# Kernel tuning notes

Measured on AMD Instinct MI355X. Metric: run time of the kernel, lower is better.

The kernel has to match this reference:

```python
import jax, jax.numpy as jnp
import numpy as np

IN_F = 4096
OUT_F = 4096
GS = 128              # group_size
GC = IN_F // GS       # group_count = 32
PACK = 8              # int4 values per int32


def setup_inputs() -> dict:
    key = jax.random.key(0)
    k1, k2, k3, k4, k5 = jax.random.split(key, 5)
    x = jax.random.normal(k1, (4, 2048, IN_F), dtype=jnp.float32)
    # packed int4 weights: (out_features, in_features // 8), nibbles in low->high bits
    qweight = jax.random.randint(k2, (OUT_F, IN_F // PACK), -(2**31), 2**31 - 1, dtype=jnp.int32)
    scales = jax.random.uniform(k3, (GC, OUT_F), dtype=jnp.float32) * 0.01
    qzeros = jax.random.randint(k4, (GC, OUT_F), 0, 16, dtype=jnp.int32)
    bias = jax.random.normal(k5, (OUT_F,), dtype=jnp.float32) * 0.01
    return {"x": x, "qweight": qweight, "scales": scales, "qzeros": qzeros, "bias": bias}


def _dequantize(qweight, scales, qzeros):
    # unpack 8 nibbles per int32 along last dim (shifts 0,4,...,28), as in _unpack_int4_last_dim
    shifts = jnp.arange(0, 32, 4, dtype=jnp.int32)  # [8]
    w_int = ((qweight[:, :, None] >> shifts) & 15)  # (OUT, IN//8, 8)
    w_int = w_int.reshape(OUT_F, IN_F).astype(jnp.float32)  # (OUT, IN)
    gid = jnp.arange(IN_F) // GS  # (IN,) group id per input channel
    z = qzeros.astype(jnp.float32)[gid].T   # (OUT, IN)
    s = scales[gid].T                        # (OUT, IN)
    return (w_int - z) * s                   # (OUT, IN)


def reference(x, qweight, scales, qzeros, bias):
    W = _dequantize(qweight, scales, qzeros)          # (OUT, IN)
    # F.linear: y = x @ W^T + b
    return jnp.einsum('bsi,oi->bso', x, W) + bias
```

## Files before the change

### kernel.cpp

```cpp
#include <hip/hip_runtime.h>
#include <hip/hip_bf16.h>
#include <stdint.h>

#define IN_F 4096
#define OUT_F 4096
#define M_TOTAL 8192
#define NKT 64

typedef __hip_bfloat16 bf16;
typedef __attribute__((ext_vector_type(8))) short bf16x8;
typedef __attribute__((ext_vector_type(4))) float f32x4;

__global__ __launch_bounds__(256) void dequant_w(const int* __restrict__ qweight,
                                                 const float* __restrict__ scales,
                                                 const int* __restrict__ qzeros,
                                                 bf16* __restrict__ Wb) {
    int idx = blockIdx.x * 256 + threadIdx.x;
    int o = idx >> 9;
    int j = idx & 511;
    int g = j >> 4;
    int qw = qweight[idx];
    float s = scales[g * OUT_F + o];
    float z = (float)qzeros[g * OUT_F + o];
    union { bf16 h[8]; uint4 q; } out;
#pragma unroll
    for (int b = 0; b < 8; ++b) {
        float w = (float)((qw >> (4 * b)) & 15);
        out.h[b] = __float2bfloat16((w - z) * s);
    }
    *reinterpret_cast<uint4*>(Wb + ((size_t)o * IN_F + j * 8)) = out.q;
}

__global__ __launch_bounds__(256) void cvt_x(const float* __restrict__ x,
                                             bf16* __restrict__ Xb, int n8) {
    int idx = blockIdx.x * 256 + threadIdx.x;
    if (idx >= n8) return;
    const float4* p = reinterpret_cast<const float4*>(x) + (size_t)idx * 2;
    float4 a = p[0], b = p[1];
    union { bf16 h[8]; uint4 q; } o;
    o.h[0] = __float2bfloat16(a.x); o.h[1] = __float2bfloat16(a.y);
    o.h[2] = __float2bfloat16(a.z); o.h[3] = __float2bfloat16(a.w);
    o.h[4] = __float2bfloat16(b.x); o.h[5] = __float2bfloat16(b.y);
    o.h[6] = __float2bfloat16(b.z); o.h[7] = __float2bfloat16(b.w);
    reinterpret_cast<uint4*>(Xb)[idx] = o.q;
}


__device__ __forceinline__ void gload16(const bf16* g, char* l) {
    __builtin_amdgcn_global_load_lds(
        (const __attribute__((address_space(1))) void*)g,
        (__attribute__((address_space(3))) void*)l, 16, 0, 0);
}

__device__ __forceinline__ void stage_half(const bf16* __restrict__ Gt,
                                           char* ldsb, int wave, int lane) {
    const int slog8 = ((lane & 7) ^ (lane >> 3)) * 8;
#pragma unroll
    for (int j = 0; j < 2; ++j) {
        int r = wave * 16 + j * 8 + (lane >> 3);
        gload16(Gt + (size_t)r * IN_F + slog8, ldsb + (wave * 2 + j) * 1024);
    }
}

#define BARRIER() do { asm volatile("" ::: "memory"); \
                       __builtin_amdgcn_s_barrier();  \
                       asm volatile("" ::: "memory"); } while (0)
#define LGKM0()   asm volatile("s_waitcnt lgkmcnt(0)" ::: "memory")
#define VMCNT4()  asm volatile("s_waitcnt vmcnt(4)" ::: "memory")
#define VMCNT0()  asm volatile("s_waitcnt vmcnt(0)" ::: "memory")

#define LDA_SET(DST, BUF, MH) do {                                              \
  _Pragma("unroll") for (int m4 = 0; m4 < 4; ++m4)                              \
  _Pragma("unroll") for (int kk = 0; kk < 2; ++kk)                              \
    DST[m4][kk] = *reinterpret_cast<const bf16x8*>(sm + (BUF) * 65536           \
        + ((wr * 128 + (MH) * 64 + m4 * 16 + l15) << 7)                         \
        + ((((kk << 2) + lq) ^ l7) << 4));                                      \
} while (0)

#define LDB_SET(BUF, NH) do {                                                   \
  _Pragma("unroll") for (int n2 = 0; n2 < 2; ++n2)                              \
  _Pragma("unroll") for (int kk = 0; kk < 2; ++kk)                              \
    bfr[n2][kk] = *reinterpret_cast<const bf16x8*>(sm + (BUF) * 65536 + 32768   \
        + ((wc * 64 + (NH) * 32 + n2 * 16 + l15) << 7)                          \
        + ((((kk << 2) + lq) ^ l7) << 4));                                      \
} while (0)

#define MMA_Q(AF, MH, NH) do {                                                  \
  __builtin_amdgcn_s_setprio(1);                                                \
  _Pragma("unroll") for (int m4 = 0; m4 < 4; ++m4)                              \
  _Pragma("unroll") for (int n2 = 0; n2 < 2; ++n2)                              \
  _Pragma("unroll") for (int kk = 0; kk < 2; ++kk)                              \
    acc[(MH) * 4 + m4][(NH) * 2 + n2] = __builtin_amdgcn_mfma_f32_16x16x32_bf16(\
        AF[m4][kk], bfr[n2][kk], acc[(MH) * 4 + m4][(NH) * 2 + n2], 0, 0, 0);   \
  __builtin_amdgcn_s_setprio(0);                                                \
} while (0)

__global__ __launch_bounds__(512, 2) void gemm256(const bf16* __restrict__ A,
                                                  const bf16* __restrict__ B,
                                                  const float* __restrict__ bias,
                                                  float* __restrict__ C) {
    extern __shared__ char sm[];
    const int tid  = threadIdx.x;
    const int wave = tid >> 6;
    const int lane = tid & 63;
    const int wr   = wave >> 2;
    const int wc   = wave & 3;
    const int l15  = lane & 15;
    const int lq   = lane >> 4;
    const int l7   = lane & 7;

    const int nwg = gridDim.x;
    const int cpx = nwg >> 3;
    const int wg  = blockIdx.x;
    const int swz = (wg & 7) * cpx + (wg >> 3);
    const int bm  = swz >> 4;
    const int bn  = swz & 15;
    const int m0  = bm * 256;
    const int n0  = bn * 256;

    f32x4 acc[8][4];
#pragma unroll
    for (int m = 0; m < 8; ++m)
#pragma unroll
        for (int n = 0; n < 4; ++n) acc[m][n] = (f32x4){0.f, 0.f, 0.f, 0.f};

    bf16x8 af0[4][2], af1[4][2], bfr[2][2];

    stage_half(A + (size_t)m0 * IN_F,                sm + 0,     wave, lane);
    stage_half(A + (size_t)(m0 + 128) * IN_F,        sm + 16384, wave, lane);
    stage_half(B + (size_t)n0 * IN_F,                sm + 32768, wave, lane);
    stage_half(B + (size_t)(n0 + 128) * IN_F,        sm + 49152, wave, lane);
    stage_half(A + (size_t)m0 * IN_F + 64,           sm + 65536, wave, lane);
    stage_half(A + (size_t)(m0 + 128) * IN_F + 64,   sm + 81920, wave, lane);
    VMCNT4();
    BARRIER();

    for (int i = 0; i < 32; ++i) {
        const int tB1 = 2 * i + 1;
        const int t2  = 2 * i + 2;
        const int t3  = 2 * i + 3;
        const bool g2 = t2 < NKT;
        const bool g3 = t3 < NKT;
        const bf16* Bk1 = B + (size_t)tB1 * 64;
        const bf16* Ak2 = A + (size_t)t2 * 64;
        const bf16* Bk2 = B + (size_t)t2 * 64;
        const bf16* Ak3 = A + (size_t)t3 * 64;

        LDA_SET(af0, 0, 0);
        LDB_SET(0, 0);
        stage_half(Bk1 + (size_t)n0 * IN_F,         sm + 98304,  wave, lane);
        BARRIER(); LGKM0();
        MMA_Q(af0, 0, 0);
        BARRIER();
        LDA_SET(af1, 0, 1);
        stage_half(Bk1 + (size_t)(n0 + 128) * IN_F, sm + 114688, wave, lane);
        BARRIER(); LGKM0();
        MMA_Q(af1, 1, 0);
        BARRIER();
        LDB_SET(0, 1);
        if (g2) stage_half(Ak2 + (size_t)m0 * IN_F,         sm + 0,     wave, lane);
        BARRIER(); LGKM0();
        MMA_Q(af0, 0, 1);
        BARRIER();
        if (g2) stage_half(Ak2 + (size_t)(m0 + 128) * IN_F, sm + 16384, wave, lane);
        BARRIER(); LGKM0();
        MMA_Q(af1, 1, 1);
        if (i < 31) { VMCNT4(); } else { VMCNT0(); }
        BARRIER();

        LDA_SET(af0, 1, 0);
        LDB_SET(1, 0);
        if (g2) stage_half(Bk2 + (size_t)n0 * IN_F,         sm + 32768, wave, lane);
        BARRIER(); LGKM0();
        MMA_Q(af0, 0, 0);
        BARRIER();
        LDA_SET(af1, 1, 1);
        if (g2) stage_half(Bk2 + (size_t)(n0 + 128) * IN_F, sm + 49152, wave, lane);
        BARRIER(); LGKM0();
        MMA_Q(af1, 1, 0);
        BARRIER();
        LDB_SET(1, 1);
        if (g3) stage_half(Ak3 + (size_t)m0 * IN_F,         sm + 65536, wave, lane);
        BARRIER(); LGKM0();
        MMA_Q(af0, 0, 1);
        BARRIER();
        if (g3) stage_half(Ak3 + (size_t)(m0 + 128) * IN_F, sm + 81920, wave, lane);
        BARRIER(); LGKM0();
        MMA_Q(af1, 1, 1);
        if (i < 31) { VMCNT4(); } else { VMCNT0(); }
        BARRIER();
    }

    const int crow0 = m0 + wr * 128 + lq * 4;
    const int ccol0 = n0 + wc * 64 + l15;
#pragma unroll
    for (int n = 0; n < 4; ++n) {
        float bv = bias[ccol0 + n * 16];
#pragma unroll
        for (int m = 0; m < 8; ++m)
#pragma unroll
            for (int r = 0; r < 4; ++r)
                C[(size_t)(crow0 + m * 16 + r) * OUT_F + ccol0 + n * 16] = acc[m][n][r] + bv;
    }
}

__global__ __launch_bounds__(256) void fallback_gemm(const float* __restrict__ x,
                                                     const int* __restrict__ qweight,
                                                     const float* __restrict__ scales,
                                                     const int* __restrict__ qzeros,
                                                     const float* __restrict__ bias,
                                                     float* __restrict__ out) {
    __shared__ float Asf[64][65];
    __shared__ float Bsf[64][65];
    int bm = blockIdx.x >> 6;
    int bn = blockIdx.x & 63;
    int m0 = bm * 64, n0 = bn * 64;
    int t  = threadIdx.x;
    int tr = t >> 4, tc = t & 15;
    float acc[4][4] = {};
    for (int kt = 0; kt < IN_F; kt += 64) {
#pragma unroll
        for (int i = 0; i < 4; ++i) {
            int idx = t + i * 256;
            int r = idx >> 4, c4 = idx & 15;
            float4 v = *reinterpret_cast<const float4*>(x + (size_t)(m0 + r) * IN_F + kt + c4 * 4);
            Asf[r][c4 * 4 + 0] = v.x; Asf[r][c4 * 4 + 1] = v.y;
            Asf[r][c4 * 4 + 2] = v.z; Asf[r][c4 * 4 + 3] = v.w;
        }
#pragma unroll
        for (int i = 0; i < 2; ++i) {
            int idx = t + i * 256;
            int r = idx >> 3, k8 = idx & 7;
            int kk = kt + k8 * 8;
            int o  = n0 + r;
            int qw = qweight[(size_t)o * (IN_F / 8) + (kk >> 3)];
            int g  = kk >> 7;
            float s = scales[g * OUT_F + o];
            float z = (float)qzeros[g * OUT_F + o];
#pragma unroll
            for (int b = 0; b < 8; ++b)
                Bsf[r][k8 * 8 + b] = ((float)((qw >> (4 * b)) & 15) - z) * s;
        }
        __syncthreads();
#pragma unroll 8
        for (int k = 0; k < 64; ++k) {
            float a[4], bb[4];
#pragma unroll
            for (int i = 0; i < 4; ++i) a[i] = Asf[tr * 4 + i][k];
#pragma unroll
            for (int j = 0; j < 4; ++j) bb[j] = Bsf[tc * 4 + j][k];
#pragma unroll
            for (int i = 0; i < 4; ++i)
#pragma unroll
                for (int j = 0; j < 4; ++j) acc[i][j] += a[i] * bb[j];
        }
        __syncthreads();
    }
#pragma unroll
    for (int i = 0; i < 4; ++i) {
        int row = m0 + tr * 4 + i;
#pragma unroll
        for (int j = 0; j < 4; ++j) {
            int col = n0 + tc * 4 + j;
            out[(size_t)row * OUT_F + col] = acc[i][j] + bias[col];
        }
    }
}

extern "C" void kernel_launch(void* const* d_in, const int* in_sizes, int n_in,
                              void* d_out, int out_size, void* d_ws, size_t ws_size,
                              hipStream_t stream) {
    (void)in_sizes; (void)n_in; (void)out_size;
    const float* x       = (const float*)d_in[0];
    const int*   qweight = (const int*)d_in[1];
    const float* scales  = (const float*)d_in[2];
    const int*   qzeros  = (const int*)d_in[3];
    const float* bias    = (const float*)d_in[4];
    float* out = (float*)d_out;

    const size_t needW = (size_t)OUT_F * IN_F * sizeof(bf16);
    const size_t needX = (size_t)M_TOTAL * IN_F * sizeof(bf16);

    if (ws_size >= needW + needX) {
        bf16* Wb = (bf16*)d_ws;
        bf16* Xb = (bf16*)((char*)d_ws + needW);
        dequant_w<<<(OUT_F * (IN_F / 8)) / 256, 256, 0, stream>>>(qweight, scales, qzeros, Wb);
        int n8 = M_TOTAL * IN_F / 8;
        cvt_x<<<(n8 + 255) / 256, 256, 0, stream>>>(x, Xb, n8);
        gemm256<<<(M_TOTAL / 256) * (OUT_F / 256), 512, 131072, stream>>>(Xb, Wb, bias, out);
    } else {
        fallback_gemm<<<(M_TOTAL / 64) * (OUT_F / 64), 256, 0, stream>>>(
            x, qweight, scales, qzeros, bias, out);
    }
}
```

Baseline: 274.3 us.

## Stage GEMM tiles by wave-quadrant units to prefetch deeper

Replaces half-tile staging with A/B staging units matched to which wave quadrant consumes them, so each load slot fills exactly the rows the next MMA phase reads. The prefetch schedule is reordered to issue loads further ahead (one extra unit in the prologue, vmcnt raised from 4 to 6), aiming to hide global-to-LDS latency behind MFMA work. The cost is more in-flight loads, and correctness depends on the new ordering of LDS buffer reuse.

```diff
diff --git a/kernel.cpp b/kernel.cpp
--- a/kernel.cpp
+++ b/kernel.cpp
@@ -52,13 +52,23 @@
         (__attribute__((address_space(3))) void*)l, 16, 0, 0);
 }
 
-__device__ __forceinline__ void stage_half(const bf16* __restrict__ Gt,
-                                           char* ldsb, int wave, int lane) {
+__device__ __forceinline__ void stage_Aunit(const bf16* __restrict__ G, char* Abase,
+                                            int MH, int wave, int lane) {
     const int slog8 = ((lane & 7) ^ (lane >> 3)) * 8;
 #pragma unroll
     for (int j = 0; j < 2; ++j) {
-        int r = wave * 16 + j * 8 + (lane >> 3);
-        gload16(Gt + (size_t)r * IN_F + slog8, ldsb + (wave * 2 + j) * 1024);
+        int rb = ((wave >> 2) << 7) + (MH << 6) + ((wave & 3) << 4) + (j << 3);
+        gload16(G + (size_t)(rb + (lane >> 3)) * IN_F + slog8, Abase + rb * 128);
+    }
+}
+
+__device__ __forceinline__ void stage_Bunit(const bf16* __restrict__ G, char* Bbase,
+                                            int NH, int wave, int lane) {
+    const int slog8 = ((lane & 7) ^ (lane >> 3)) * 8;
+#pragma unroll
+    for (int j = 0; j < 2; ++j) {
+        int rb = ((wave >> 1) << 6) + (NH << 5) + ((wave & 1) << 4) + (j << 3);
+        gload16(G + (size_t)(rb + (lane >> 3)) * IN_F + slog8, Bbase + rb * 128);
     }
 }
 
@@ -66,7 +76,7 @@
                        __builtin_amdgcn_s_barrier();  \
                        asm volatile("" ::: "memory"); } while (0)
 #define LGKM0()   asm volatile("s_waitcnt lgkmcnt(0)" ::: "memory")
-#define VMCNT4()  asm volatile("s_waitcnt vmcnt(4)" ::: "memory")
+#define VMCNT6()  asm volatile("s_waitcnt vmcnt(6)" ::: "memory")
 #define VMCNT0()  asm volatile("s_waitcnt vmcnt(0)" ::: "memory")
 
 #define LDA_SET(DST, BUF, MH) do {                                              \
@@ -118,6 +128,14 @@
     const int m0  = bm * 256;
     const int n0  = bn * 256;
 
+    const bf16* Arow = A + (size_t)m0 * IN_F;
+    const bf16* Brow = B + (size_t)n0 * IN_F;
+
+    char* buf0A = sm;
+    char* buf0B = sm + 32768;
+    char* buf1A = sm + 65536;
+    char* buf1B = sm + 98304;
+
     f32x4 acc[8][4];
 #pragma unroll
     for (int m = 0; m < 8; ++m)
@@ -126,68 +144,69 @@
 
     bf16x8 af0[4][2], af1[4][2], bfr[2][2];
 
-    stage_half(A + (size_t)m0 * IN_F,                sm + 0,     wave, lane);
-    stage_half(A + (size_t)(m0 + 128) * IN_F,        sm + 16384, wave, lane);
-    stage_half(B + (size_t)n0 * IN_F,                sm + 32768, wave, lane);
-    stage_half(B + (size_t)(n0 + 128) * IN_F,        sm + 49152, wave, lane);
-    stage_half(A + (size_t)m0 * IN_F + 64,           sm + 65536, wave, lane);
-    stage_half(A + (size_t)(m0 + 128) * IN_F + 64,   sm + 81920, wave, lane);
-    VMCNT4();
+    stage_Aunit(Arow,       buf0A, 0, wave, lane);
+    stage_Aunit(Arow,       buf0A, 1, wave, lane);
+    stage_Bunit(Brow,       buf0B, 0, wave, lane);
+    stage_Bunit(Brow,       buf0B, 1, wave, lane);
+    stage_Aunit(Arow + 64,  buf1A, 0, wave, lane);
+    stage_Aunit(Arow + 64,  buf1A, 1, wave, lane);
+    stage_Bunit(Brow + 64,  buf1B, 0, wave, lane);
+    VMCNT6();
     BARRIER();
 
     for (int i = 0; i < 32; ++i) {
-        const int tB1 = 2 * i + 1;
-        const int t2  = 2 * i + 2;
-        const int t3  = 2 * i + 3;
-        const bool g2 = t2 < NKT;
-        const bool g3 = t3 < NKT;
-        const bf16* Bk1 = B + (size_t)tB1 * 64;
-        const bf16* Ak2 = A + (size_t)t2 * 64;
-        const bf16* Bk2 = B + (size_t)t2 * 64;
-        const bf16* Ak3 = A + (size_t)t3 * 64;
+        const int t1 = 2 * i + 1;
+        const int t2 = 2 * i + 2;
+        const int t3 = 2 * i + 3;
+        const bool gg = (i < 31);
+        const bf16* At2 = Arow + t2 * 64;
+        const bf16* Bt2 = Brow + t2 * 64;
+        const bf16* At3 = Arow + t3 * 64;
+        const bf16* Bt1 = Brow + t1 * 64;
+        const bf16* Bt3 = Brow + t3 * 64;
 
         LDA_SET(af0, 0, 0);
         LDB_SET(0, 0);
-        stage_half(Bk1 + (size_t)n0 * IN_F,         sm + 98304,  wave, lane);
+        stage_Bunit(Bt1, buf1B, 1, wave, lane);
         BARRIER(); LGKM0();
         MMA_Q(af0, 0, 0);
         BARRIER();
         LDA_SET(af1, 0, 1);
-        stage_half(Bk1 + (size_t)(n0 + 128) * IN_F, sm + 114688, wave, lane);
+        if (gg) stage_Aunit(At2, buf0A, 0, wave, lane);
         BARRIER(); LGKM0();
         MMA_Q(af1, 1, 0);
         BARRIER();
         LDB_SET(0, 1);
-        if (g2) stage_half(Ak2 + (size_t)m0 * IN_F,         sm + 0,     wave, lane);
+        if (gg) stage_Aunit(At2, buf0A, 1, wave, lane);
         BARRIER(); LGKM0();
         MMA_Q(af0, 0, 1);
         BARRIER();
-        if (g2) stage_half(Ak2 + (size_t)(m0 + 128) * IN_F, sm + 16384, wave, lane);
+        if (gg) stage_Bunit(Bt2, buf0B, 0, wave, lane);
         BARRIER(); LGKM0();
         MMA_Q(af1, 1, 1);
-        if (i < 31) { VMCNT4(); } else { VMCNT0(); }
+        if (gg) { VMCNT6(); } else { VMCNT0(); }
         BARRIER();
 
         LDA_SET(af0, 1, 0);
         LDB_SET(1, 0);
-        if (g2) stage_half(Bk2 + (size_t)n0 * IN_F,         sm + 32768, wave, lane);
+        if (gg) stage_Bunit(Bt2, buf0B, 1, wave, lane);
         BARRIER(); LGKM0();
         MMA_Q(af0, 0, 0);
         BARRIER();
         LDA_SET(af1, 1, 1);
-        if (g2) stage_half(Bk2 + (size_t)(n0 + 128) * IN_F, sm + 49152, wave, lane);
+        if (gg) stage_Aunit(At3, buf1A, 0, wave, lane);
         BARRIER(); LGKM0();
         MMA_Q(af1, 1, 0);
         BARRIER();
         LDB_SET(1, 1);
-        if (g3) stage_half(Ak3 + (size_t)m0 * IN_F,         sm + 65536, wave, lane);
+        if (gg) stage_Aunit(At3, buf1A, 1, wave, lane);
         BARRIER(); LGKM0();
         MMA_Q(af0, 0, 1);
         BARRIER();
-        if (g3) stage_half(Ak3 + (size_t)(m0 + 128) * IN_F, sm + 81920, wave, lane);
+        if (gg) stage_Bunit(Bt3, buf1B, 0, wave, lane);
         BARRIER(); LGKM0();
         MMA_Q(af1, 1, 1);
-        if (i < 31) { VMCNT4(); } else { VMCNT0(); }
+        if (gg) { VMCNT6(); } else { VMCNT0(); }
         BARRIER();
     }
 
```

New measurement: 539.5 us. +96.7%, slower.

## Remap wave tiles across LDS halves and deepen prefetch by one stage

Applied to the files above, without the earlier changes.

Each wave's A and B subtiles are remapped so that its quadrant rows are interleaved across the two 128-row staged halves, which changes which LDS half each MMA phase depends on. With that mapping, the B-half loads are issued one phase earlier, so a seventh stage is prefetched and the wait threshold rises from 4 to 6 outstanding loads. The aim is to hide more global-load latency behind the MFMA phases. The epilogue row and column mapping is updated to match, and the tail-guard logic is simplified to a single flag.

```diff
diff --git a/kernel.cpp b/kernel.cpp
--- a/kernel.cpp
+++ b/kernel.cpp
@@ -66,14 +66,14 @@
                        __builtin_amdgcn_s_barrier();  \
                        asm volatile("" ::: "memory"); } while (0)
 #define LGKM0()   asm volatile("s_waitcnt lgkmcnt(0)" ::: "memory")
-#define VMCNT4()  asm volatile("s_waitcnt vmcnt(4)" ::: "memory")
+#define VMCNT6()  asm volatile("s_waitcnt vmcnt(6)" ::: "memory")
 #define VMCNT0()  asm volatile("s_waitcnt vmcnt(0)" ::: "memory")
 
 #define LDA_SET(DST, BUF, MH) do {                                              \
   _Pragma("unroll") for (int m4 = 0; m4 < 4; ++m4)                              \
   _Pragma("unroll") for (int kk = 0; kk < 2; ++kk)                              \
     DST[m4][kk] = *reinterpret_cast<const bf16x8*>(sm + (BUF) * 65536           \
-        + ((wr * 128 + (MH) * 64 + m4 * 16 + l15) << 7)                         \
+        + (((MH) * 128 + wr * 64 + m4 * 16 + l15) << 7)                         \
         + ((((kk << 2) + lq) ^ l7) << 4));                                      \
 } while (0)
 
@@ -81,7 +81,7 @@
   _Pragma("unroll") for (int n2 = 0; n2 < 2; ++n2)                              \
   _Pragma("unroll") for (int kk = 0; kk < 2; ++kk)                              \
     bfr[n2][kk] = *reinterpret_cast<const bf16x8*>(sm + (BUF) * 65536 + 32768   \
-        + ((wc * 64 + (NH) * 32 + n2 * 16 + l15) << 7)                          \
+        + (((NH) * 128 + wc * 32 + n2 * 16 + l15) << 7)                         \
         + ((((kk << 2) + lq) ^ l7) << 4));                                      \
 } while (0)
 
@@ -118,6 +118,11 @@
     const int m0  = bm * 256;
     const int n0  = bn * 256;
 
+    const bf16* A0 = A + (size_t)m0 * IN_F;
+    const bf16* A1 = A + (size_t)(m0 + 128) * IN_F;
+    const bf16* B0 = B + (size_t)n0 * IN_F;
+    const bf16* B1 = B + (size_t)(n0 + 128) * IN_F;
+
     f32x4 acc[8][4];
 #pragma unroll
     for (int m = 0; m < 8; ++m)
@@ -126,81 +131,82 @@
 
     bf16x8 af0[4][2], af1[4][2], bfr[2][2];
 
-    stage_half(A + (size_t)m0 * IN_F,                sm + 0,     wave, lane);
-    stage_half(A + (size_t)(m0 + 128) * IN_F,        sm + 16384, wave, lane);
-    stage_half(B + (size_t)n0 * IN_F,                sm + 32768, wave, lane);
-    stage_half(B + (size_t)(n0 + 128) * IN_F,        sm + 49152, wave, lane);
-    stage_half(A + (size_t)m0 * IN_F + 64,           sm + 65536, wave, lane);
-    stage_half(A + (size_t)(m0 + 128) * IN_F + 64,   sm + 81920, wave, lane);
-    VMCNT4();
+    stage_half(A0,      sm + 0,     wave, lane);
+    stage_half(A1,      sm + 16384, wave, lane);
+    stage_half(B0,      sm + 32768, wave, lane);
+    stage_half(B1,      sm + 49152, wave, lane);
+    stage_half(A0 + 64, sm + 65536, wave, lane);
+    stage_half(A1 + 64, sm + 81920, wave, lane);
+    stage_half(B0 + 64, sm + 98304, wave, lane);
+    VMCNT6();
     BARRIER();
 
     for (int i = 0; i < 32; ++i) {
-        const int tB1 = 2 * i + 1;
-        const int t2  = 2 * i + 2;
-        const int t3  = 2 * i + 3;
-        const bool g2 = t2 < NKT;
-        const bool g3 = t3 < NKT;
-        const bf16* Bk1 = B + (size_t)tB1 * 64;
-        const bf16* Ak2 = A + (size_t)t2 * 64;
-        const bf16* Bk2 = B + (size_t)t2 * 64;
-        const bf16* Ak3 = A + (size_t)t3 * 64;
+        const int t1 = 2 * i + 1;
+        const int t2 = 2 * i + 2;
+        const int t3 = 2 * i + 3;
+        const bool gg = (i < 31);
 
         LDA_SET(af0, 0, 0);
         LDB_SET(0, 0);
-        stage_half(Bk1 + (size_t)n0 * IN_F,         sm + 98304,  wave, lane);
+        stage_half(B1 + t1 * 64, sm + 114688, wave, lane);
         BARRIER(); LGKM0();
         MMA_Q(af0, 0, 0);
         BARRIER();
         LDA_SET(af1, 0, 1);
-        stage_half(Bk1 + (size_t)(n0 + 128) * IN_F, sm + 114688, wave, lane);
+        if (gg) stage_half(A0 + t2 * 64, sm + 0, wave, lane);
         BARRIER(); LGKM0();
         MMA_Q(af1, 1, 0);
         BARRIER();
         LDB_SET(0, 1);
-        if (g2) stage_half(Ak2 + (size_t)m0 * IN_F,         sm + 0,     wave, lane);
+        if (gg) stage_half(A1 + t2 * 64, sm + 16384, wave, lane);
         BARRIER(); LGKM0();
         MMA_Q(af0, 0, 1);
         BARRIER();
-        if (g2) stage_half(Ak2 + (size_t)(m0 + 128) * IN_F, sm + 16384, wave, lane);
+        if (gg) stage_half(B0 + t2 * 64, sm + 32768, wave, lane);
         BARRIER(); LGKM0();
         MMA_Q(af1, 1, 1);
-        if (i < 31) { VMCNT4(); } else { VMCNT0(); }
+        if (gg) { VMCNT6(); } else { VMCNT0(); }
         BARRIER();
 
         LDA_SET(af0, 1, 0);
         LDB_SET(1, 0);
-        if (g2) stage_half(Bk2 + (size_t)n0 * IN_F,         sm + 32768, wave, lane);
+        if (gg) stage_half(B1 + t2 * 64, sm + 49152, wave, lane);
         BARRIER(); LGKM0();
         MMA_Q(af0, 0, 0);
         BARRIER();
         LDA_SET(af1, 1, 1);
-        if (g2) stage_half(Bk2 + (size_t)(n0 + 128) * IN_F, sm + 49152, wave, lane);
+        if (gg) stage_half(A0 + t3 * 64, sm + 65536, wave, lane);
         BARRIER(); LGKM0();
         MMA_Q(af1, 1, 0);
         BARRIER();
         LDB_SET(1, 1);
-        if (g3) stage_half(Ak3 + (size_t)m0 * IN_F,         sm + 65536, wave, lane);
+        if (gg) stage_half(A1 + t3 * 64, sm + 81920, wave, lane);
         BARRIER(); LGKM0();
         MMA_Q(af0, 0, 1);
         BARRIER();
-        if (g3) stage_half(Ak3 + (size_t)(m0 + 128) * IN_F, sm + 81920, wave, lane);
+        if (gg) stage_half(B0 + t3 * 64, sm + 98304, wave, lane);
         BARRIER(); LGKM0();
         MMA_Q(af1, 1, 1);
-        if (i < 31) { VMCNT4(); } else { VMCNT0(); }
-        BARRIER();
-    }
-
-    const int crow0 = m0 + wr * 128 + lq * 4;
-    const int ccol0 = n0 + wc * 64 + l15;
+        if (gg) { VMCNT6(); } else { VMCNT0(); }
+        BARRIER();
+    }
+
+    const int crow_base = m0 + wr * 64 + lq * 4;
+    const int ccol_base = n0 + wc * 32 + l15;
 #pragma unroll
     for (int n = 0; n < 4; ++n) {
-        float bv = bias[ccol0 + n * 16];
-#pragma unroll
-        for (int m = 0; m < 8; ++m)
+        const int NH = n >> 1, n2 = n & 1;
+        const int col = ccol_base + NH * 128 + n2 * 16;
+        float bv = bias[col];
+#pragma unroll
+        for (int m = 0; m < 8; ++m) {
+            const int MH = m >> 2, m4 = m & 3;
+            const int row = crow_base + MH * 128 + m4 * 16;
 #pragma unroll
             for (int r = 0; r < 4; ++r)
-                C[(size_t)(crow0 + m * 16 + r) * OUT_F + ccol0 + n * 16] = acc[m][n][r] + bv;
+                C[(size_t)(row + r) * OUT_F + col] = acc[m][n][r] + bv;
+        }
     }
 }
 
```

Measured after the change: 274.3 us. About the same (+0.0%).
